# Performance work log

Hardware: AMD Instinct MI355X
Metric: run time of the kernel (lower is better)

The kernel has to match this reference:

```python
import jax, jax.numpy as jnp
import numpy as np


def setup_inputs() -> dict:
    key = jax.random.key(0)
    k1, k2, k3, k4 = jax.random.split(key, 4)
    B, L, D_IN, D_OUT, E = 512, 50, 768, 300, 8
    x = jax.random.normal(k1, (B, L, D_IN), dtype=jnp.float32)
    w_gate = jax.random.normal(k2, (D_IN, E), dtype=jnp.float32) * 0.02
    expert_w = jax.random.normal(k3, (E, D_OUT, D_IN), dtype=jnp.float32) * 0.02
    expert_bias = jax.random.normal(k4, (E, L, D_IN), dtype=jnp.float32) * 0.02
    return {"x": x, "w_gate": w_gate, "expert_w": expert_w, "expert_bias": expert_bias}


def reference(x, w_gate, expert_w, expert_bias):
    # Gating (eval mode: noisy gating disabled) -> softmax over experts
    gates = jax.nn.softmax(x @ w_gate, axis=-1)  # [B, L, E]
    # DTRLayer: lin(x - bias) = x @ W^T - bias @ W^T (linearity avoids [B,L,E,D_in] intermediate)
    xw = jnp.einsum('bli,eoi->bleo', x, expert_w)           # [B, L, E, O]
    bw = jnp.einsum('eli,eoi->leo', expert_bias, expert_w)  # [L, E, O]
    expert_out = xw - bw[None]                              # [B, L, E, O]
    # Gate-weighted sum over experts
    return jnp.einsum('ble,bleo->blo', gates, expert_out)   # [B, L, O]
```

## Files before the change

kernel.cpp:

```cpp
#include <hip/hip_runtime.h>
#include <hip/hip_bf16.h>

#define BATCH   512
#define LSEQ    50
#define DIN     768
#define DOUT    300
#define NEXP    8
#define NTOK    (BATCH * LSEQ)

typedef __bf16 bf16_t;
typedef __attribute__((ext_vector_type(8))) __bf16 bf16x8;
typedef __attribute__((ext_vector_type(4))) float f32x4;

#define GLDS16(g, l) __builtin_amdgcn_global_load_lds( \
    (__attribute__((address_space(1))) void*)(g), \
    (__attribute__((address_space(3))) void*)(l), 16, 0, 0)

static __device__ __forceinline__ unsigned short f2bf(float f) {
    unsigned u = __float_as_uint(f);
    u = (u + 0x7fff + ((u >> 16) & 1)) >> 16;
    return (unsigned short)u;
}

#define PREP_GATE_BLOCKS (NTOK / 4)
#define PREP_BW_BLOCKS   ((2 * NEXP * DOUT) / 4)

__global__ __launch_bounds__(256) void prep_kernel(
    const float* __restrict__ x, const float* __restrict__ wg,
    const float* __restrict__ bias, const float* __restrict__ W,
    unsigned short* __restrict__ xb, float* __restrict__ gates,
    float* __restrict__ bw, unsigned short* __restrict__ wb)
{
    const int tid  = threadIdx.x;
    const int lane = tid & 63;

    if (blockIdx.x < PREP_GATE_BLOCKS) {
        __shared__ float wgT[NEXP][DIN + 4];
        #pragma unroll
        for (int r = 0; r < 6; ++r) {
            int j = tid + 256 * r;
            float4 v = ((const float4*)wg)[j];
            int i  = j >> 1;
            int e0 = (j & 1) * 4;
            wgT[e0 + 0][i] = v.x;
            wgT[e0 + 1][i] = v.y;
            wgT[e0 + 2][i] = v.z;
            wgT[e0 + 3][i] = v.w;
        }
        __syncthreads();

        int t = blockIdx.x * 4 + (tid >> 6);
        const float4* xr = (const float4*)(x + (size_t)t * DIN);
        ushort4* xo = (ushort4*)(xb + (size_t)t * DIN);

        float acc[NEXP];
        #pragma unroll
        for (int e = 0; e < NEXP; e++) acc[e] = 0.0f;

        #pragma unroll
        for (int k = 0; k < 3; ++k) {
            int i4 = lane + 64 * k;
            float4 v = xr[i4];
            ushort4 u;
            u.x = f2bf(v.x); u.y = f2bf(v.y); u.z = f2bf(v.z); u.w = f2bf(v.w);
            xo[i4] = u;
            #pragma unroll
            for (int e = 0; e < NEXP; ++e) {
                float4 wv = *(const float4*)&wgT[e][4 * i4];
                acc[e] += v.x * wv.x + v.y * wv.y + v.z * wv.z + v.w * wv.w;
            }
        }
        #pragma unroll
        for (int e = 0; e < NEXP; e++) {
            #pragma unroll
            for (int m = 32; m > 0; m >>= 1) acc[e] += __shfl_xor(acc[e], m, 64);
        }
        float mx = acc[0];
        #pragma unroll
        for (int e = 1; e < NEXP; e++) mx = fmaxf(mx, acc[e]);
        float ex[NEXP]; float s = 0.0f;
        #pragma unroll
        for (int e = 0; e < NEXP; e++) { ex[e] = __expf(acc[e] - mx); s += ex[e]; }
        float inv = 1.0f / s;
        if (lane == 0) {
            #pragma unroll
            for (int e = 0; e < NEXP; e++) gates[(size_t)t * NEXP + e] = ex[e] * inv;
        }
    } else {
        int wid  = (blockIdx.x - PREP_GATE_BLOCKS) * 4 + (tid >> 6);
        int half = wid & 1;
        int eo   = wid >> 1;
        int e = eo / DOUT, o = eo % DOUT;

        const float4* wr = (const float4*)(W + ((size_t)e * DOUT + o) * DIN);
        float4 w4[3];
        #pragma unroll
        for (int k = 0; k < 3; ++k) w4[k] = wr[lane + 64 * k];

        if (half == 0) {
            ushort4* wo = (ushort4*)(wb + ((size_t)e * DOUT + o) * DIN);
            #pragma unroll
            for (int k = 0; k < 3; ++k) {
                ushort4 u;
                u.x = f2bf(w4[k].x); u.y = f2bf(w4[k].y);
                u.z = f2bf(w4[k].z); u.w = f2bf(w4[k].w);
                wo[lane + 64 * k] = u;
            }
        }

        int l0 = 25 * half;
        for (int l = l0; l < l0 + 25; ++l) {
            const float4* br = (const float4*)(bias + ((size_t)e * LSEQ + l) * DIN);
            float acc = 0.0f;
            #pragma unroll
            for (int k = 0; k < 3; ++k) {
                float4 b = br[lane + 64 * k];
                acc += b.x * w4[k].x + b.y * w4[k].y + b.z * w4[k].z + b.w * w4[k].w;
            }
            #pragma unroll
            for (int m = 32; m > 0; m >>= 1) acc += __shfl_xor(acc, m, 64);
            if (lane == 0) bw[((size_t)l * NEXP + e) * DOUT + o] = acc;
        }
    }
}

#define GTM 256
#define GTO 16
#define GBK 32
#define GKIT (DIN / GBK)
#define NRT  (NTOK / GTM)
#define NOT  19
#define RPG  13

__global__ __launch_bounds__(256, 2) void moe_mfma_kernel(
    const bf16_t* __restrict__ xb, const bf16_t* __restrict__ wb,
    const float* __restrict__ gates, const float* __restrict__ bw,
    float* __restrict__ out)
{
    const int bid  = blockIdx.x;
    const int g    = bid & 7;
    const int slot = bid >> 3;
    const int r_in = slot / NOT;
    const int o_t  = slot - NOT * r_in;
    const int r_t  = g * RPG + r_in;
    if (r_t >= NRT) return;
    const int o0 = o_t * GTO;
    const int t0 = r_t * GTM;

    __shared__ f32x4 ldsv[1536];
    char* Xs = (char*)ldsv;
    char* Ws = (char*)ldsv + 16384;

    const int tid  = threadIdx.x;
    const int w    = tid >> 6;
    const int lane = tid & 63;

    const int srow4 = lane >> 2;
    const int c16   = 16 * ((lane & 3) ^ ((lane >> 4) & 3));

    const char* xg[4];
    #pragma unroll
    for (int j = 0; j < 4; ++j)
        xg[j] = (const char*)xb + (size_t)(t0 + 64 * w + 16 * j + srow4) * (DIN * 2) + c16;
    char* xl = Xs + 4096 * w;

    const char* wg[2];
    #pragma unroll
    for (int j = 0; j < 2; ++j) {
        int n = 32 * w + 16 * j + srow4;
        int e = n >> 4;
        int o = o0 + (n & 15); if (o >= DOUT) o = DOUT - 1;
        wg[j] = (const char*)wb + (size_t)(e * DOUT + o) * (DIN * 2) + c16;
    }
    char* wl = Ws + 2048 * w;

    const int m = lane & 15, q = lane >> 4;
    const int sw = 16 * (q ^ ((m >> 2) & 3));
    int aoff[4], boff[8];
    #pragma unroll
    for (int rf = 0; rf < 4; ++rf) aoff[rf] = 64 * (64 * w + 16 * rf + m) + sw;
    #pragma unroll
    for (int cf = 0; cf < 8; ++cf) boff[cf] = 64 * (16 * cf + m) + sw;

    f32x4 acc[4][8] = {};

    for (int it = 0; it < GKIT; ++it) {
        #pragma unroll
        for (int j = 0; j < 4; ++j) GLDS16(xg[j], xl + 1024 * j);
        #pragma unroll
        for (int j = 0; j < 2; ++j) GLDS16(wg[j], wl + 1024 * j);
        #pragma unroll
        for (int j = 0; j < 4; ++j) xg[j] += 64;
        #pragma unroll
        for (int j = 0; j < 2; ++j) wg[j] += 64;
        __syncthreads();

        bf16x8 a[4];
        #pragma unroll
        for (int rf = 0; rf < 4; ++rf) a[rf] = *(const bf16x8*)(Xs + aoff[rf]);
        #pragma unroll
        for (int cf = 0; cf < 8; ++cf) {
            bf16x8 b = *(const bf16x8*)(Ws + boff[cf]);
            #pragma unroll
            for (int rf = 0; rf < 4; ++rf)
                acc[rf][cf] = __builtin_amdgcn_mfma_f32_16x16x32_bf16(a[rf], b, acc[rf][cf], 0, 0, 0);
        }
        __syncthreads();
    }

    const int o = o0 + m;
    if (o < DOUT) {
        #pragma unroll
        for (int rf = 0; rf < 4; ++rf) {
            #pragma unroll
            for (int r = 0; r < 4; ++r) {
                int t = t0 + 64 * w + 16 * rf + 4 * q + r;
                int l = t % LSEQ;
                float4 g0 = *(const float4*)(gates + (size_t)t * NEXP);
                float4 g1 = *(const float4*)(gates + (size_t)t * NEXP + 4);
                const float* bp = bw + (size_t)l * NEXP * DOUT + o;
                float s = 0.0f;
                s += g0.x * (acc[rf][0][r] - bp[0 * DOUT]);
                s += g0.y * (acc[rf][1][r] - bp[1 * DOUT]);
                s += g0.z * (acc[rf][2][r] - bp[2 * DOUT]);
                s += g0.w * (acc[rf][3][r] - bp[3 * DOUT]);
                s += g1.x * (acc[rf][4][r] - bp[4 * DOUT]);
                s += g1.y * (acc[rf][5][r] - bp[5 * DOUT]);
                s += g1.z * (acc[rf][6][r] - bp[6 * DOUT]);
                s += g1.w * (acc[rf][7][r] - bp[7 * DOUT]);
                out[(size_t)t * DOUT + o] = s;
            }
        }
    }
}

__global__ __launch_bounds__(256) void gates_kernel(
    const float* __restrict__ x, const float* __restrict__ wg,
    float* __restrict__ gates)
{
    int t    = blockIdx.x * 4 + (threadIdx.x >> 6);
    int lane = threadIdx.x & 63;
    const float* xr = x + (size_t)t * DIN;
    float acc[NEXP];
    #pragma unroll
    for (int e = 0; e < NEXP; e++) acc[e] = 0.0f;
    for (int i = lane; i < DIN; i += 64) {
        float xv = xr[i];
        const float* wr = wg + (size_t)i * NEXP;
        #pragma unroll
        for (int e = 0; e < NEXP; e++) acc[e] += xv * wr[e];
    }
    #pragma unroll
    for (int e = 0; e < NEXP; e++) {
        #pragma unroll
        for (int m = 32; m > 0; m >>= 1) acc[e] += __shfl_xor(acc[e], m, 64);
    }
    float mx = acc[0];
    #pragma unroll
    for (int e = 1; e < NEXP; e++) mx = fmaxf(mx, acc[e]);
    float ex[NEXP]; float s = 0.0f;
    #pragma unroll
    for (int e = 0; e < NEXP; e++) { ex[e] = __expf(acc[e] - mx); s += ex[e]; }
    float inv = 1.0f / s;
    if (lane == 0) {
        #pragma unroll
        for (int e = 0; e < NEXP; e++) gates[(size_t)t * NEXP + e] = ex[e] * inv;
    }
}

__global__ __launch_bounds__(256) void bw_kernel(
    const float* __restrict__ bias, const float* __restrict__ W,
    float* __restrict__ bw)
{
    int wave = blockIdx.x * 4 + (threadIdx.x >> 6);
    int lane = threadIdx.x & 63;
    int l   = wave / (NEXP * DOUT);
    int rem = wave % (NEXP * DOUT);
    int e   = rem / DOUT;
    int o   = rem % DOUT;
    const float4* br = (const float4*)(bias + ((size_t)e * LSEQ + l) * DIN);
    const float4* wr = (const float4*)(W    + ((size_t)e * DOUT + o) * DIN);
    float acc = 0.0f;
    #pragma unroll
    for (int k = 0; k < 3; ++k) {
        int i4 = lane + 64 * k;
        float4 b = br[i4], w = wr[i4];
        acc += b.x * w.x + b.y * w.y + b.z * w.z + b.w * w.w;
    }
    #pragma unroll
    for (int m = 32; m > 0; m >>= 1) acc += __shfl_xor(acc, m, 64);
    if (lane == 0) bw[((size_t)l * NEXP + e) * DOUT + o] = acc;
}

#define TM  64
#define TO  16
#define KT  32
#define KTP 36

__global__ __launch_bounds__(256) void moe_main_kernel(
    const float* __restrict__ x, const float* __restrict__ W,
    const float* __restrict__ gates, const float* __restrict__ bw,
    float* __restrict__ out)
{
    __shared__ float Xs[TM][KTP];
    __shared__ float Wls[128][KTP];
    const int tid = threadIdx.x;
    const int t0 = blockIdx.x * TM;
    const int o0 = blockIdx.y * TO;
    const int cg = tid & 15;
    const int tg = tid >> 4;
    const int lrow = tid >> 3;
    const int lk4  = (tid & 7) * 4;
    float acc[4][NEXP];
    #pragma unroll
    for (int i = 0; i < 4; i++)
        #pragma unroll
        for (int j = 0; j < NEXP; j++) acc[i][j] = 0.0f;
    for (int k0 = 0; k0 < DIN; k0 += KT) {
        #pragma unroll
        for (int r = 0; r < 2; r++) {
            int row = lrow + 32 * r;
            float4 v = *(const float4*)&x[((size_t)(t0 + row)) * DIN + k0 + lk4];
            *(float4*)&Xs[row][lk4] = v;
        }
        #pragma unroll
        for (int r = 0; r < 4; r++) {
            int nl = lrow + 32 * r;
            int e  = nl >> 4;
            int o  = o0 + (nl & 15);
            float4 v;
            if (o < DOUT)
                v = *(const float4*)&W[((size_t)e * DOUT + o) * DIN + k0 + lk4];
            else
                v = make_float4(0.f, 0.f, 0.f, 0.f);
            *(float4*)&Wls[nl][lk4] = v;
        }
        __syncthreads();
        #pragma unroll
        for (int k4 = 0; k4 < KT; k4 += 4) {
            float4 xa[4], wb4[NEXP];
            #pragma unroll
            for (int i = 0; i < 4; i++)
                xa[i] = *(const float4*)&Xs[tg + 16 * i][k4];
            #pragma unroll
            for (int j = 0; j < NEXP; j++)
                wb4[j] = *(const float4*)&Wls[cg + 16 * j][k4];
            #pragma unroll
            for (int i = 0; i < 4; i++)
                #pragma unroll
                for (int j = 0; j < NEXP; j++) {
                    acc[i][j] += xa[i].x * wb4[j].x;
                    acc[i][j] += xa[i].y * wb4[j].y;
                    acc[i][j] += xa[i].z * wb4[j].z;
                    acc[i][j] += xa[i].w * wb4[j].w;
                }
        }
        __syncthreads();
    }
    const int o = o0 + cg;
    if (o < DOUT) {
        #pragma unroll
        for (int i = 0; i < 4; i++) {
            int t = t0 + tg + 16 * i;
            int l = t % LSEQ;
            float s = 0.0f;
            #pragma unroll
            for (int j = 0; j < NEXP; j++) {
                float g = gates[(size_t)t * NEXP + j];
                s += g * (acc[i][j] - bw[((size_t)l * NEXP + j) * DOUT + o]);
            }
            out[(size_t)t * DOUT + o] = s;
        }
    }
}

extern "C" void kernel_launch(void* const* d_in, const int* in_sizes, int n_in,
                              void* d_out, int out_size, void* d_ws, size_t ws_size,
                              hipStream_t stream) {
    const float* x     = (const float*)d_in[0];
    const float* wgate = (const float*)d_in[1];
    const float* ew    = (const float*)d_in[2];
    const float* ebias = (const float*)d_in[3];
    float* out = (float*)d_out;

    const size_t n_gates = (size_t)NTOK * NEXP;
    const size_t n_bw    = (size_t)LSEQ * NEXP * DOUT;
    const size_t n_x     = (size_t)NTOK * DIN;
    const size_t n_w     = (size_t)NEXP * DOUT * DIN;

    float* gates = (float*)d_ws;
    float* bw    = gates + n_gates;
    bf16_t* xb   = (bf16_t*)(bw + n_bw);
    bf16_t* wbuf = xb + n_x;

    const size_t need = (n_gates + n_bw) * 4 + (n_x + n_w) * 2;

    if (ws_size >= need) {
        prep_kernel<<<PREP_GATE_BLOCKS + PREP_BW_BLOCKS, 256, 0, stream>>>(
            x, wgate, ebias, ew, (unsigned short*)xb, gates, bw, (unsigned short*)wbuf);
        moe_mfma_kernel<<<8 * RPG * NOT, 256, 0, stream>>>(xb, wbuf, gates, bw, out);
    } else {
        gates_kernel<<<NTOK / 4, 256, 0, stream>>>(x, wgate, gates);
        bw_kernel<<<(LSEQ * NEXP * DOUT) / 4, 256, 0, stream>>>(ebias, ew, bw);
        dim3 grid(NTOK / TM, (DOUT + TO - 1) / TO);
        moe_main_kernel<<<grid, 256, 0, stream>>>(x, ew, gates, bw, out);
    }
}
```

Before: 267.4 us.

## Fuse prep and MFMA GEMM into one cooperative persistent kernel with grid sync

Merges the gating/bf16-conversion/bias-projection prep stage and the bf16 MFMA GEMM into a single cooperative kernel of 512 persistent blocks. A grid-wide sync separates the two phases, and both phases iterate over work units with grid-stride loops. The goal is to remove the second kernel launch and the gap between kernels. The cost is a grid barrier, possible load imbalance from the fixed grid size, and fewer blocks in flight during the GEMM phase than the previous 1976-block launch. If the cooperative launch fails, the code falls back to the original two-kernel path.

```diff
diff --git a/kernel.cpp b/kernel.cpp
--- a/kernel.cpp
+++ b/kernel.cpp
@@ -1,5 +1,8 @@
 #include <hip/hip_runtime.h>
 #include <hip/hip_bf16.h>
+#include <hip/hip_cooperative_groups.h>
+
+namespace cg = cooperative_groups;
 
 #define BATCH   512
 #define LSEQ    50
@@ -20,6 +23,226 @@
     unsigned u = __float_as_uint(f);
     u = (u + 0x7fff + ((u >> 16) & 1)) >> 16;
     return (unsigned short)u;
+}
+
+#define GTM 256
+#define GTO 16
+#define GBK 32
+#define GKIT (DIN / GBK)
+#define NRT  (NTOK / GTM)
+#define NOT  19
+#define RPG  13
+#define NSLOT (8 * RPG * NOT)
+
+#define FUSED_GRID 512
+#define NUNITS (6400 + 4800)
+
+__global__ __launch_bounds__(256, 2) void fused_moe_kernel(
+    const float* __restrict__ x, const float* __restrict__ wgp,
+    const float* __restrict__ bias, const float* __restrict__ W,
+    unsigned short* __restrict__ xbu, float* __restrict__ gates,
+    float* __restrict__ bw, unsigned short* __restrict__ wbu,
+    float* __restrict__ out)
+{
+    __shared__ __align__(16) float wgT[NEXP][DIN + 4];
+
+    const int tid  = threadIdx.x;
+    const int lane = tid & 63;
+    const int w    = tid >> 6;
+
+    #pragma unroll
+    for (int r = 0; r < 6; ++r) {
+        int j = tid + 256 * r;
+        float4 v = ((const float4*)wgp)[j];
+        int i  = j >> 1;
+        int e0 = (j & 1) * 4;
+        wgT[e0 + 0][i] = v.x;
+        wgT[e0 + 1][i] = v.y;
+        wgT[e0 + 2][i] = v.z;
+        wgT[e0 + 3][i] = v.w;
+    }
+    __syncthreads();
+
+    const int gw = blockIdx.x * 4 + w;
+    for (int u = gw; u < NUNITS; u += FUSED_GRID * 4) {
+        if (u < 6400) {
+            const int tb = u * 4;
+            for (int tk = 0; tk < 4; ++tk) {
+                const int t = tb + tk;
+                const float4* xr = (const float4*)(x + (size_t)t * DIN);
+                ushort4*      xo = (ushort4*)(xbu + (size_t)t * DIN);
+
+                float acc[NEXP];
+                #pragma unroll
+                for (int e = 0; e < NEXP; e++) acc[e] = 0.0f;
+
+                #pragma unroll
+                for (int k = 0; k < 3; ++k) {
+                    int i4 = lane + 64 * k;
+                    float4 v = xr[i4];
+                    ushort4 uu;
+                    uu.x = f2bf(v.x); uu.y = f2bf(v.y);
+                    uu.z = f2bf(v.z); uu.w = f2bf(v.w);
+                    xo[i4] = uu;
+                    #pragma unroll
+                    for (int e = 0; e < NEXP; ++e) {
+                        float4 wv = *(const float4*)&wgT[e][4 * i4];
+                        acc[e] += v.x * wv.x + v.y * wv.y + v.z * wv.z + v.w * wv.w;
+                    }
+                }
+                #pragma unroll
+                for (int e = 0; e < NEXP; e++) {
+                    #pragma unroll
+                    for (int m2 = 32; m2 > 0; m2 >>= 1)
+                        acc[e] += __shfl_xor(acc[e], m2, 64);
+                }
+                float mx = acc[0];
+                #pragma unroll
+                for (int e = 1; e < NEXP; e++) mx = fmaxf(mx, acc[e]);
+                float ex[NEXP]; float s = 0.0f;
+                #pragma unroll
+                for (int e = 0; e < NEXP; e++) { ex[e] = __expf(acc[e] - mx); s += ex[e]; }
+                float inv = 1.0f / s;
+                if (lane == 0) {
+                    *(float4*)(gates + (size_t)t * NEXP) =
+                        make_float4(ex[0]*inv, ex[1]*inv, ex[2]*inv, ex[3]*inv);
+                    *(float4*)(gates + (size_t)t * NEXP + 4) =
+                        make_float4(ex[4]*inv, ex[5]*inv, ex[6]*inv, ex[7]*inv);
+                }
+            }
+        } else {
+            const int wid  = u - 6400;
+            const int half = wid & 1;
+            const int eo   = wid >> 1;
+            const int e = eo / DOUT, o = eo % DOUT;
+
+            const float4* wr = (const float4*)(W + ((size_t)e * DOUT + o) * DIN);
+            float4 w4[3];
+            #pragma unroll
+            for (int k = 0; k < 3; ++k) w4[k] = wr[lane + 64 * k];
+
+            if (half == 0) {
+                ushort4* wo = (ushort4*)(wbu + ((size_t)e * DOUT + o) * DIN);
+                #pragma unroll
+                for (int k = 0; k < 3; ++k) {
+                    ushort4 uu;
+                    uu.x = f2bf(w4[k].x); uu.y = f2bf(w4[k].y);
+                    uu.z = f2bf(w4[k].z); uu.w = f2bf(w4[k].w);
+                    wo[lane + 64 * k] = uu;
+                }
+            }
+
+            int l0 = 25 * half;
+            for (int l = l0; l < l0 + 25; ++l) {
+                const float4* br = (const float4*)(bias + ((size_t)e * LSEQ + l) * DIN);
+                float acc = 0.0f;
+                #pragma unroll
+                for (int k = 0; k < 3; ++k) {
+                    float4 b = br[lane + 64 * k];
+                    acc += b.x * w4[k].x + b.y * w4[k].y + b.z * w4[k].z + b.w * w4[k].w;
+                }
+                #pragma unroll
+                for (int m2 = 32; m2 > 0; m2 >>= 1) acc += __shfl_xor(acc, m2, 64);
+                if (lane == 0) bw[((size_t)l * NEXP + e) * DOUT + o] = acc;
+            }
+        }
+    }
+
+    cg::this_grid().sync();
+
+    char* Xs = (char*)wgT;
+    char* Ws = (char*)wgT + 16384;
+
+    const int srow4 = lane >> 2;
+    const int c16   = 16 * ((lane & 3) ^ ((lane >> 4) & 3));
+    const int m = lane & 15, q = lane >> 4;
+    const int sw = 16 * (q ^ ((m >> 2) & 3));
+    int aoff[4], boff[8];
+    #pragma unroll
+    for (int rf = 0; rf < 4; ++rf) aoff[rf] = 64 * (64 * w + 16 * rf + m) + sw;
+    #pragma unroll
+    for (int cf = 0; cf < 8; ++cf) boff[cf] = 64 * (16 * cf + m) + sw;
+
+    const bf16_t* xb = (const bf16_t*)xbu;
+    const bf16_t* wb = (const bf16_t*)wbu;
+
+    for (int vb = blockIdx.x; vb < NSLOT; vb += FUSED_GRID) {
+        const int g    = vb & 7;
+        const int slot = vb >> 3;
+        const int r_in = slot / NOT;
+        const int o_t  = slot - NOT * r_in;
+        const int r_t  = g * RPG + r_in;
+        if (r_t >= NRT) continue;
+        const int o0 = o_t * GTO;
+        const int t0 = r_t * GTM;
+
+        const char* xg[4];
+        #pragma unroll
+        for (int j = 0; j < 4; ++j)
+            xg[j] = (const char*)xb + (size_t)(t0 + 64 * w + 16 * j + srow4) * (DIN * 2) + c16;
+        char* xl = Xs + 4096 * w;
+
+        const char* wq[2];
+        #pragma unroll
+        for (int j = 0; j < 2; ++j) {
+            int n = 32 * w + 16 * j + srow4;
+            int e = n >> 4;
+            int o = o0 + (n & 15); if (o >= DOUT) o = DOUT - 1;
+            wq[j] = (const char*)wb + (size_t)(e * DOUT + o) * (DIN * 2) + c16;
+        }
+        char* wl = Ws + 2048 * w;
+
+        f32x4 acc[4][8] = {};
+
+        for (int it = 0; it < GKIT; ++it) {
+            #pragma unroll
+            for (int j = 0; j < 4; ++j) GLDS16(xg[j], xl + 1024 * j);
+            #pragma unroll
+            for (int j = 0; j < 2; ++j) GLDS16(wq[j], wl + 1024 * j);
+            #pragma unroll
+            for (int j = 0; j < 4; ++j) xg[j] += 64;
+            #pragma unroll
+            for (int j = 0; j < 2; ++j) wq[j] += 64;
+            __syncthreads();
+
+            bf16x8 a[4];
+            #pragma unroll
+            for (int rf = 0; rf < 4; ++rf) a[rf] = *(const bf16x8*)(Xs + aoff[rf]);
+            #pragma unroll
+            for (int cf = 0; cf < 8; ++cf) {
+                bf16x8 b = *(const bf16x8*)(Ws + boff[cf]);
+                #pragma unroll
+                for (int rf = 0; rf < 4; ++rf)
+                    acc[rf][cf] = __builtin_amdgcn_mfma_f32_16x16x32_bf16(a[rf], b, acc[rf][cf], 0, 0, 0);
+            }
+            __syncthreads();
+        }
+
+        const int o = o0 + m;
+        if (o < DOUT) {
+            #pragma unroll
+            for (int rf = 0; rf < 4; ++rf) {
+                #pragma unroll
+                for (int r = 0; r < 4; ++r) {
+                    int t = t0 + 64 * w + 16 * rf + 4 * q + r;
+                    int l = t % LSEQ;
+                    float4 g0 = *(const float4*)(gates + (size_t)t * NEXP);
+                    float4 g1 = *(const float4*)(gates + (size_t)t * NEXP + 4);
+                    const float* bp = bw + (size_t)l * NEXP * DOUT + o;
+                    float s = 0.0f;
+                    s += g0.x * (acc[rf][0][r] - bp[0 * DOUT]);
+                    s += g0.y * (acc[rf][1][r] - bp[1 * DOUT]);
+                    s += g0.z * (acc[rf][2][r] - bp[2 * DOUT]);
+                    s += g0.w * (acc[rf][3][r] - bp[3 * DOUT]);
+                    s += g1.x * (acc[rf][4][r] - bp[4 * DOUT]);
+                    s += g1.y * (acc[rf][5][r] - bp[5 * DOUT]);
+                    s += g1.z * (acc[rf][6][r] - bp[6 * DOUT]);
+                    s += g1.w * (acc[rf][7][r] - bp[7 * DOUT]);
+                    out[(size_t)t * DOUT + o] = s;
+                }
+            }
+        }
+    }
 }
 
 #define PREP_GATE_BLOCKS (NTOK / 4)
@@ -123,14 +346,6 @@
         }
     }
 }
-
-#define GTM 256
-#define GTO 16
-#define GBK 32
-#define GKIT (DIN / GBK)
-#define NRT  (NTOK / GTM)
-#define NOT  19
-#define RPG  13
 
 __global__ __launch_bounds__(256, 2) void moe_mfma_kernel(
     const bf16_t* __restrict__ xb, const bf16_t* __restrict__ wb,
@@ -307,7 +522,7 @@
     const int tid = threadIdx.x;
     const int t0 = blockIdx.x * TM;
     const int o0 = blockIdx.y * TO;
-    const int cg = tid & 15;
+    const int cg2 = tid & 15;
     const int tg = tid >> 4;
     const int lrow = tid >> 3;
     const int lk4  = (tid & 7) * 4;
@@ -344,7 +559,7 @@
                 xa[i] = *(const float4*)&Xs[tg + 16 * i][k4];
             #pragma unroll
             for (int j = 0; j < NEXP; j++)
-                wb4[j] = *(const float4*)&Wls[cg + 16 * j][k4];
+                wb4[j] = *(const float4*)&Wls[cg2 + 16 * j][k4];
             #pragma unroll
             for (int i = 0; i < 4; i++)
                 #pragma unroll
@@ -357,7 +572,7 @@
         }
         __syncthreads();
     }
-    const int o = o0 + cg;
+    const int o = o0 + cg2;
     if (o < DOUT) {
         #pragma unroll
         for (int i = 0; i < 4; i++) {
@@ -396,9 +611,19 @@
     const size_t need = (n_gates + n_bw) * 4 + (n_x + n_w) * 2;
 
     if (ws_size >= need) {
-        prep_kernel<<<PREP_GATE_BLOCKS + PREP_BW_BLOCKS, 256, 0, stream>>>(
-            x, wgate, ebias, ew, (unsigned short*)xb, gates, bw, (unsigned short*)wbuf);
-        moe_mfma_kernel<<<8 * RPG * NOT, 256, 0, stream>>>(xb, wbuf, gates, bw, out);
+        unsigned short* xbu = (unsigned short*)xb;
+        unsigned short* wbu = (unsigned short*)wbuf;
+        void* kargs[] = {
+            (void*)&x, (void*)&wgate, (void*)&ebias, (void*)&ew,
+            (void*)&xbu, (void*)&gates, (void*)&bw, (void*)&wbu, (void*)&out
+        };
+        hipError_t cerr = hipLaunchCooperativeKernel(
+            fused_moe_kernel, dim3(FUSED_GRID), dim3(256), kargs, 0u, stream);
+        if (cerr != hipSuccess) {
+            prep_kernel<<<PREP_GATE_BLOCKS + PREP_BW_BLOCKS, 256, 0, stream>>>(
+                x, wgate, ebias, ew, (unsigned short*)xb, gates, bw, (unsigned short*)wbuf);
+            moe_mfma_kernel<<<NSLOT, 256, 0, stream>>>(xb, wbuf, gates, bw, out);
+        }
     } else {
         gates_kernel<<<NTOK / 4, 256, 0, stream>>>(x, wgate, gates);
         bw_kernel<<<(LSEQ * NEXP * DOUT) / 4, 256, 0, stream>>>(ebias, ew, bw);
```

After: 379.6 us. +42.0%, slower.

## Use 512-thread blocks with triple-buffered LDS pipeline in MoE MFMA GEMM

Applied to the files above, without the earlier changes.

Replaces the 256-thread, single-buffered GEMM loop with a 512-thread block covering 512 tokens, a three-stage LDS ring (prefetch two K-steps ahead) and split load/compute phases with explicit waitcnt, barriers and setprio. The aim is to hide global-to-LDS latency behind MFMA work and halve redundant weight-tile loads per token. In exchange it needs 120KB of LDS per block, which may limit occupancy, and relies on exact vmcnt accounting for correctness. The epilogue is unchanged apart from the indexing rework.

```diff
diff --git a/kernel.cpp b/kernel.cpp
--- a/kernel.cpp
+++ b/kernel.cpp
@@ -124,15 +124,15 @@
     }
 }
 
-#define GTM 256
-#define GTO 16
-#define GBK 32
-#define GKIT (DIN / GBK)
-#define NRT  (NTOK / GTM)
-#define NOT  19
-#define RPG  13
-
-__global__ __launch_bounds__(256, 2) void moe_mfma_kernel(
+#define BM8   512
+#define NRT8  (NTOK / BM8)
+#define NOT8  19
+#define RPG8  7
+#define NSLOT8 (8 * RPG8 * NOT8)
+#define KTN   (DIN / 32)
+#define TBUF  40960
+
+__global__ __launch_bounds__(512, 2) void moe_mfma8_kernel(
     const bf16_t* __restrict__ xb, const bf16_t* __restrict__ wb,
     const float* __restrict__ gates, const float* __restrict__ bw,
     float* __restrict__ out)
@@ -140,16 +140,14 @@
     const int bid  = blockIdx.x;
     const int g    = bid & 7;
     const int slot = bid >> 3;
-    const int r_in = slot / NOT;
-    const int o_t  = slot - NOT * r_in;
-    const int r_t  = g * RPG + r_in;
-    if (r_t >= NRT) return;
-    const int o0 = o_t * GTO;
-    const int t0 = r_t * GTM;
-
-    __shared__ f32x4 ldsv[1536];
-    char* Xs = (char*)ldsv;
-    char* Ws = (char*)ldsv + 16384;
+    const int r_in = slot / NOT8;
+    const int o_t  = slot - NOT8 * r_in;
+    const int r_t  = g * RPG8 + r_in;
+    if (r_t >= NRT8) return;
+    const int o0 = o_t * 16;
+    const int t0 = r_t * BM8;
+
+    __shared__ __align__(16) char lds[3 * TBUF];
 
     const int tid  = threadIdx.x;
     const int w    = tid >> 6;
@@ -158,54 +156,110 @@
     const int srow4 = lane >> 2;
     const int c16   = 16 * ((lane & 3) ^ ((lane >> 4) & 3));
 
-    const char* xg[4];
-    #pragma unroll
-    for (int j = 0; j < 4; ++j)
-        xg[j] = (const char*)xb + (size_t)(t0 + 64 * w + 16 * j + srow4) * (DIN * 2) + c16;
-    char* xl = Xs + 4096 * w;
-
-    const char* wg[2];
-    #pragma unroll
-    for (int j = 0; j < 2; ++j) {
-        int n = 32 * w + 16 * j + srow4;
+    const char* xga[4];
+    #pragma unroll
+    for (int r = 0; r < 4; ++r)
+        xga[r] = (const char*)xb + (size_t)(t0 + r * 128 + w * 16 + srow4) * (DIN * 2) + c16;
+
+    const char* wga;
+    {
+        int n = w * 16 + srow4;
         int e = n >> 4;
         int o = o0 + (n & 15); if (o >= DOUT) o = DOUT - 1;
-        wg[j] = (const char*)wb + (size_t)(e * DOUT + o) * (DIN * 2) + c16;
-    }
-    char* wl = Ws + 2048 * w;
+        wga = (const char*)wb + (size_t)(e * DOUT + o) * (DIN * 2) + c16;
+    }
 
     const int m = lane & 15, q = lane >> 4;
     const int sw = 16 * (q ^ ((m >> 2) & 3));
     int aoff[4], boff[8];
     #pragma unroll
-    for (int rf = 0; rf < 4; ++rf) aoff[rf] = 64 * (64 * w + 16 * rf + m) + sw;
-    #pragma unroll
-    for (int cf = 0; cf < 8; ++cf) boff[cf] = 64 * (16 * cf + m) + sw;
+    for (int rf = 0; rf < 4; ++rf) aoff[rf] = (w * 64 + rf * 16 + m) * 64 + sw;
+    #pragma unroll
+    for (int cf = 0; cf < 8; ++cf) boff[cf] = 32768 + (cf * 16 + m) * 64 + sw;
 
     f32x4 acc[4][8] = {};
 
-    for (int it = 0; it < GKIT; ++it) {
-        #pragma unroll
-        for (int j = 0; j < 4; ++j) GLDS16(xg[j], xl + 1024 * j);
-        #pragma unroll
-        for (int j = 0; j < 2; ++j) GLDS16(wg[j], wl + 1024 * j);
-        #pragma unroll
-        for (int j = 0; j < 4; ++j) xg[j] += 64;
-        #pragma unroll
-        for (int j = 0; j < 2; ++j) wg[j] += 64;
-        __syncthreads();
-
-        bf16x8 a[4];
-        #pragma unroll
-        for (int rf = 0; rf < 4; ++rf) a[rf] = *(const bf16x8*)(Xs + aoff[rf]);
-        #pragma unroll
-        for (int cf = 0; cf < 8; ++cf) {
-            bf16x8 b = *(const bf16x8*)(Ws + boff[cf]);
-            #pragma unroll
-            for (int rf = 0; rf < 4; ++rf)
-                acc[rf][cf] = __builtin_amdgcn_mfma_f32_16x16x32_bf16(a[rf], b, acc[rf][cf], 0, 0, 0);
-        }
-        __syncthreads();
+    #pragma unroll
+    for (int r = 0; r < 4; ++r) GLDS16(xga[r], lds + r * 8192 + w * 1024);
+    GLDS16(wga, lds + 32768 + w * 1024);
+    #pragma unroll
+    for (int r = 0; r < 4; ++r) GLDS16(xga[r] + 64, lds + TBUF + r * 8192 + w * 1024);
+    GLDS16(wga + 64, lds + TBUF + 32768 + w * 1024);
+
+    int cbuf = 0;
+    for (int j = 0; j < KTN; ++j) {
+        int s = j + 2; if (s >= KTN) s -= KTN;
+        const int koff = s * 64;
+        int sbuf = cbuf + 2; if (sbuf >= 3) sbuf -= 3;
+        char* sb = lds + sbuf * TBUF;
+        const char* cb = lds + cbuf * TBUF;
+
+        GLDS16(xga[0] + koff, sb + 0 * 8192 + w * 1024);
+        GLDS16(xga[1] + koff, sb + 1 * 8192 + w * 1024);
+        GLDS16(xga[2] + koff, sb + 2 * 8192 + w * 1024);
+        asm volatile("s_waitcnt vmcnt(8)" ::: "memory");
+        __builtin_amdgcn_s_barrier();
+        __builtin_amdgcn_sched_barrier(0);
+
+        bf16x8 b0 = *(const bf16x8*)(cb + boff[0]);
+        bf16x8 b1 = *(const bf16x8*)(cb + boff[1]);
+        bf16x8 b2 = *(const bf16x8*)(cb + boff[2]);
+        bf16x8 b3 = *(const bf16x8*)(cb + boff[3]);
+        bf16x8 b4 = *(const bf16x8*)(cb + boff[4]);
+        bf16x8 b5 = *(const bf16x8*)(cb + boff[5]);
+        bf16x8 b6 = *(const bf16x8*)(cb + boff[6]);
+        bf16x8 b7 = *(const bf16x8*)(cb + boff[7]);
+        bf16x8 a0 = *(const bf16x8*)(cb + aoff[0]);
+        bf16x8 a1 = *(const bf16x8*)(cb + aoff[1]);
+        asm volatile("s_waitcnt lgkmcnt(0)" ::: "memory");
+        __builtin_amdgcn_sched_barrier(0);
+        __builtin_amdgcn_s_setprio(1);
+        acc[0][0] = __builtin_amdgcn_mfma_f32_16x16x32_bf16(a0, b0, acc[0][0], 0, 0, 0);
+        acc[0][1] = __builtin_amdgcn_mfma_f32_16x16x32_bf16(a0, b1, acc[0][1], 0, 0, 0);
+        acc[0][2] = __builtin_amdgcn_mfma_f32_16x16x32_bf16(a0, b2, acc[0][2], 0, 0, 0);
+        acc[0][3] = __builtin_amdgcn_mfma_f32_16x16x32_bf16(a0, b3, acc[0][3], 0, 0, 0);
+        acc[0][4] = __builtin_amdgcn_mfma_f32_16x16x32_bf16(a0, b4, acc[0][4], 0, 0, 0);
+        acc[0][5] = __builtin_amdgcn_mfma_f32_16x16x32_bf16(a0, b5, acc[0][5], 0, 0, 0);
+        acc[0][6] = __builtin_amdgcn_mfma_f32_16x16x32_bf16(a0, b6, acc[0][6], 0, 0, 0);
+        acc[0][7] = __builtin_amdgcn_mfma_f32_16x16x32_bf16(a0, b7, acc[0][7], 0, 0, 0);
+        acc[1][0] = __builtin_amdgcn_mfma_f32_16x16x32_bf16(a1, b0, acc[1][0], 0, 0, 0);
+        acc[1][1] = __builtin_amdgcn_mfma_f32_16x16x32_bf16(a1, b1, acc[1][1], 0, 0, 0);
+        acc[1][2] = __builtin_amdgcn_mfma_f32_16x16x32_bf16(a1, b2, acc[1][2], 0, 0, 0);
+        acc[1][3] = __builtin_amdgcn_mfma_f32_16x16x32_bf16(a1, b3, acc[1][3], 0, 0, 0);
+        acc[1][4] = __builtin_amdgcn_mfma_f32_16x16x32_bf16(a1, b4, acc[1][4], 0, 0, 0);
+        acc[1][5] = __builtin_amdgcn_mfma_f32_16x16x32_bf16(a1, b5, acc[1][5], 0, 0, 0);
+        acc[1][6] = __builtin_amdgcn_mfma_f32_16x16x32_bf16(a1, b6, acc[1][6], 0, 0, 0);
+        acc[1][7] = __builtin_amdgcn_mfma_f32_16x16x32_bf16(a1, b7, acc[1][7], 0, 0, 0);
+        __builtin_amdgcn_s_setprio(0);
+        __builtin_amdgcn_s_barrier();
+
+        GLDS16(xga[3] + koff, sb + 3 * 8192 + w * 1024);
+        GLDS16(wga + koff, sb + 32768 + w * 1024);
+        bf16x8 a2 = *(const bf16x8*)(cb + aoff[2]);
+        bf16x8 a3 = *(const bf16x8*)(cb + aoff[3]);
+        asm volatile("s_waitcnt lgkmcnt(0)" ::: "memory");
+        __builtin_amdgcn_sched_barrier(0);
+        __builtin_amdgcn_s_setprio(1);
+        acc[2][0] = __builtin_amdgcn_mfma_f32_16x16x32_bf16(a2, b0, acc[2][0], 0, 0, 0);
+        acc[2][1] = __builtin_amdgcn_mfma_f32_16x16x32_bf16(a2, b1, acc[2][1], 0, 0, 0);
+        acc[2][2] = __builtin_amdgcn_mfma_f32_16x16x32_bf16(a2, b2, acc[2][2], 0, 0, 0);
+        acc[2][3] = __builtin_amdgcn_mfma_f32_16x16x32_bf16(a2, b3, acc[2][3], 0, 0, 0);
+        acc[2][4] = __builtin_amdgcn_mfma_f32_16x16x32_bf16(a2, b4, acc[2][4], 0, 0, 0);
+        acc[2][5] = __builtin_amdgcn_mfma_f32_16x16x32_bf16(a2, b5, acc[2][5], 0, 0, 0);
+        acc[2][6] = __builtin_amdgcn_mfma_f32_16x16x32_bf16(a2, b6, acc[2][6], 0, 0, 0);
+        acc[2][7] = __builtin_amdgcn_mfma_f32_16x16x32_bf16(a2, b7, acc[2][7], 0, 0, 0);
+        acc[3][0] = __builtin_amdgcn_mfma_f32_16x16x32_bf16(a3, b0, acc[3][0], 0, 0, 0);
+        acc[3][1] = __builtin_amdgcn_mfma_f32_16x16x32_bf16(a3, b1, acc[3][1], 0, 0, 0);
+        acc[3][2] = __builtin_amdgcn_mfma_f32_16x16x32_bf16(a3, b2, acc[3][2], 0, 0, 0);
+        acc[3][3] = __builtin_amdgcn_mfma_f32_16x16x32_bf16(a3, b3, acc[3][3], 0, 0, 0);
+        acc[3][4] = __builtin_amdgcn_mfma_f32_16x16x32_bf16(a3, b4, acc[3][4], 0, 0, 0);
+        acc[3][5] = __builtin_amdgcn_mfma_f32_16x16x32_bf16(a3, b5, acc[3][5], 0, 0, 0);
+        acc[3][6] = __builtin_amdgcn_mfma_f32_16x16x32_bf16(a3, b6, acc[3][6], 0, 0, 0);
+        acc[3][7] = __builtin_amdgcn_mfma_f32_16x16x32_bf16(a3, b7, acc[3][7], 0, 0, 0);
+        __builtin_amdgcn_s_setprio(0);
+        __builtin_amdgcn_s_barrier();
+
+        cbuf += 1; if (cbuf >= 3) cbuf -= 3;
     }
 
     const int o = o0 + m;
@@ -398,7 +452,7 @@
     if (ws_size >= need) {
         prep_kernel<<<PREP_GATE_BLOCKS + PREP_BW_BLOCKS, 256, 0, stream>>>(
             x, wgate, ebias, ew, (unsigned short*)xb, gates, bw, (unsigned short*)wbuf);
-        moe_mfma_kernel<<<8 * RPG * NOT, 256, 0, stream>>>(xb, wbuf, gates, bw, out);
+        moe_mfma8_kernel<<<NSLOT8, 512, 0, stream>>>(xb, wbuf, gates, bw, out);
     } else {
         gates_kernel<<<NTOK / 4, 256, 0, stream>>>(x, wgate, gates);
         bw_kernel<<<(LSEQ * NEXP * DOUT) / 4, 256, 0, stream>>>(ebias, ew, bw);
```

New measurement: 296.3 us. 10.8% more time.

## Load A fragments directly to registers and double-buffer W tiles in LDS

Applied to the files above, without the earlier changes.

The X (A operand) tile now goes straight from global memory into registers, with register double-buffering, instead of being staged through LDS. The W (B operand) tile is double-buffered in LDS, so the load for the next k-step is issued while the current step's MFMAs run. This cuts the two barriers per iteration to one and shrinks LDS use, aiming to hide global-load latency behind compute. In exchange it relies on hand-placed waitcnt and sched_barrier calls, and the direct global loads of A may be less coalesced than the LDS-staged path.

```diff
diff --git a/kernel.cpp b/kernel.cpp
--- a/kernel.cpp
+++ b/kernel.cpp
@@ -126,11 +126,81 @@
 
 #define GTM 256
 #define GTO 16
-#define GBK 32
-#define GKIT (DIN / GBK)
+#define GKIT (DIN / 32)
 #define NRT  (NTOK / GTM)
 #define NOT  19
 #define RPG  13
+#define NSLOT (8 * RPG * NOT)
+#define BBUF 8192
+
+#define MFMA32(A0, A1, A2, A3)                                                      \
+    acc[0][0] = __builtin_amdgcn_mfma_f32_16x16x32_bf16(A0, b0, acc[0][0], 0, 0, 0); \
+    acc[0][1] = __builtin_amdgcn_mfma_f32_16x16x32_bf16(A0, b1, acc[0][1], 0, 0, 0); \
+    acc[0][2] = __builtin_amdgcn_mfma_f32_16x16x32_bf16(A0, b2, acc[0][2], 0, 0, 0); \
+    acc[0][3] = __builtin_amdgcn_mfma_f32_16x16x32_bf16(A0, b3, acc[0][3], 0, 0, 0); \
+    acc[0][4] = __builtin_amdgcn_mfma_f32_16x16x32_bf16(A0, b4, acc[0][4], 0, 0, 0); \
+    acc[0][5] = __builtin_amdgcn_mfma_f32_16x16x32_bf16(A0, b5, acc[0][5], 0, 0, 0); \
+    acc[0][6] = __builtin_amdgcn_mfma_f32_16x16x32_bf16(A0, b6, acc[0][6], 0, 0, 0); \
+    acc[0][7] = __builtin_amdgcn_mfma_f32_16x16x32_bf16(A0, b7, acc[0][7], 0, 0, 0); \
+    acc[1][0] = __builtin_amdgcn_mfma_f32_16x16x32_bf16(A1, b0, acc[1][0], 0, 0, 0); \
+    acc[1][1] = __builtin_amdgcn_mfma_f32_16x16x32_bf16(A1, b1, acc[1][1], 0, 0, 0); \
+    acc[1][2] = __builtin_amdgcn_mfma_f32_16x16x32_bf16(A1, b2, acc[1][2], 0, 0, 0); \
+    acc[1][3] = __builtin_amdgcn_mfma_f32_16x16x32_bf16(A1, b3, acc[1][3], 0, 0, 0); \
+    acc[1][4] = __builtin_amdgcn_mfma_f32_16x16x32_bf16(A1, b4, acc[1][4], 0, 0, 0); \
+    acc[1][5] = __builtin_amdgcn_mfma_f32_16x16x32_bf16(A1, b5, acc[1][5], 0, 0, 0); \
+    acc[1][6] = __builtin_amdgcn_mfma_f32_16x16x32_bf16(A1, b6, acc[1][6], 0, 0, 0); \
+    acc[1][7] = __builtin_amdgcn_mfma_f32_16x16x32_bf16(A1, b7, acc[1][7], 0, 0, 0); \
+    acc[2][0] = __builtin_amdgcn_mfma_f32_16x16x32_bf16(A2, b0, acc[2][0], 0, 0, 0); \
+    acc[2][1] = __builtin_amdgcn_mfma_f32_16x16x32_bf16(A2, b1, acc[2][1], 0, 0, 0); \
+    acc[2][2] = __builtin_amdgcn_mfma_f32_16x16x32_bf16(A2, b2, acc[2][2], 0, 0, 0); \
+    acc[2][3] = __builtin_amdgcn_mfma_f32_16x16x32_bf16(A2, b3, acc[2][3], 0, 0, 0); \
+    acc[2][4] = __builtin_amdgcn_mfma_f32_16x16x32_bf16(A2, b4, acc[2][4], 0, 0, 0); \
+    acc[2][5] = __builtin_amdgcn_mfma_f32_16x16x32_bf16(A2, b5, acc[2][5], 0, 0, 0); \
+    acc[2][6] = __builtin_amdgcn_mfma_f32_16x16x32_bf16(A2, b6, acc[2][6], 0, 0, 0); \
+    acc[2][7] = __builtin_amdgcn_mfma_f32_16x16x32_bf16(A2, b7, acc[2][7], 0, 0, 0); \
+    acc[3][0] = __builtin_amdgcn_mfma_f32_16x16x32_bf16(A3, b0, acc[3][0], 0, 0, 0); \
+    acc[3][1] = __builtin_amdgcn_mfma_f32_16x16x32_bf16(A3, b1, acc[3][1], 0, 0, 0); \
+    acc[3][2] = __builtin_amdgcn_mfma_f32_16x16x32_bf16(A3, b2, acc[3][2], 0, 0, 0); \
+    acc[3][3] = __builtin_amdgcn_mfma_f32_16x16x32_bf16(A3, b3, acc[3][3], 0, 0, 0); \
+    acc[3][4] = __builtin_amdgcn_mfma_f32_16x16x32_bf16(A3, b4, acc[3][4], 0, 0, 0); \
+    acc[3][5] = __builtin_amdgcn_mfma_f32_16x16x32_bf16(A3, b5, acc[3][5], 0, 0, 0); \
+    acc[3][6] = __builtin_amdgcn_mfma_f32_16x16x32_bf16(A3, b6, acc[3][6], 0, 0, 0); \
+    acc[3][7] = __builtin_amdgcn_mfma_f32_16x16x32_bf16(A3, b7, acc[3][7], 0, 0, 0);
+
+#define KBODY(J, AU0, AU1, AU2, AU3, AL0, AL1, AL2, AL3) do {                  \
+    const int jj  = (J);                                                       \
+    const int cur = jj & 1;                                                    \
+    if (jj + 1 < GKIT) {                                                       \
+        AL0 = *(const bf16x8*)(xga[0]);                                        \
+        AL1 = *(const bf16x8*)(xga[1]);                                        \
+        AL2 = *(const bf16x8*)(xga[2]);                                        \
+        AL3 = *(const bf16x8*)(xga[3]);                                        \
+        xga[0] += 64; xga[1] += 64; xga[2] += 64; xga[3] += 64;                \
+        asm volatile("s_waitcnt vmcnt(4)" ::: "memory");         \
+    } else {                                                                   \
+        asm volatile("s_waitcnt vmcnt(0)" ::: "memory");       \
+    }                                                                          \
+    __builtin_amdgcn_s_barrier();             \
+    __builtin_amdgcn_sched_barrier(0);                                         \
+    if (jj + 1 < GKIT) {                                                       \
+        char* nb = lds + BBUF * (cur ^ 1);                                     \
+        GLDS16(wq[0], nb + 2048 * w);                                          \
+        GLDS16(wq[1], nb + 2048 * w + 1024);                                   \
+        wq[0] += 64; wq[1] += 64;                                              \
+    }                                                                          \
+    const char* cb = lds + BBUF * cur;                                         \
+    bf16x8 b0 = *(const bf16x8*)(cb + boff[0]);                                \
+    bf16x8 b1 = *(const bf16x8*)(cb + boff[1]);                                \
+    bf16x8 b2 = *(const bf16x8*)(cb + boff[2]);                                \
+    bf16x8 b3 = *(const bf16x8*)(cb + boff[3]);                                \
+    bf16x8 b4 = *(const bf16x8*)(cb + boff[4]);                                \
+    bf16x8 b5 = *(const bf16x8*)(cb + boff[5]);                                \
+    bf16x8 b6 = *(const bf16x8*)(cb + boff[6]);                                \
+    bf16x8 b7 = *(const bf16x8*)(cb + boff[7]);                                \
+    asm volatile("s_waitcnt lgkmcnt(0)" ::: "memory");                         \
+    __builtin_amdgcn_sched_barrier(0);                                         \
+    MFMA32(AU0, AU1, AU2, AU3)                                                 \
+} while (0)
 
 __global__ __launch_bounds__(256, 2) void moe_mfma_kernel(
     const bf16_t* __restrict__ xb, const bf16_t* __restrict__ wb,
@@ -147,9 +217,7 @@
     const int o0 = o_t * GTO;
     const int t0 = r_t * GTM;
 
-    __shared__ f32x4 ldsv[1536];
-    char* Xs = (char*)ldsv;
-    char* Ws = (char*)ldsv + 16384;
+    __shared__ __align__(16) char lds[2 * BBUF];
 
     const int tid  = threadIdx.x;
     const int w    = tid >> 6;
@@ -158,54 +226,42 @@
     const int srow4 = lane >> 2;
     const int c16   = 16 * ((lane & 3) ^ ((lane >> 4) & 3));
 
-    const char* xg[4];
-    #pragma unroll
-    for (int j = 0; j < 4; ++j)
-        xg[j] = (const char*)xb + (size_t)(t0 + 64 * w + 16 * j + srow4) * (DIN * 2) + c16;
-    char* xl = Xs + 4096 * w;
-
-    const char* wg[2];
+    const char* wq[2];
     #pragma unroll
     for (int j = 0; j < 2; ++j) {
         int n = 32 * w + 16 * j + srow4;
         int e = n >> 4;
         int o = o0 + (n & 15); if (o >= DOUT) o = DOUT - 1;
-        wg[j] = (const char*)wb + (size_t)(e * DOUT + o) * (DIN * 2) + c16;
-    }
-    char* wl = Ws + 2048 * w;
+        wq[j] = (const char*)wb + (size_t)(e * DOUT + o) * (DIN * 2) + c16;
+    }
 
     const int m = lane & 15, q = lane >> 4;
     const int sw = 16 * (q ^ ((m >> 2) & 3));
-    int aoff[4], boff[8];
-    #pragma unroll
-    for (int rf = 0; rf < 4; ++rf) aoff[rf] = 64 * (64 * w + 16 * rf + m) + sw;
-    #pragma unroll
-    for (int cf = 0; cf < 8; ++cf) boff[cf] = 64 * (16 * cf + m) + sw;
+    int boff[8];
+    #pragma unroll
+    for (int cf = 0; cf < 8; ++cf) boff[cf] = (16 * cf + m) * 64 + sw;
+
+    const char* xga[4];
+    #pragma unroll
+    for (int rf = 0; rf < 4; ++rf)
+        xga[rf] = (const char*)xb + (size_t)(t0 + 64 * w + 16 * rf + m) * (DIN * 2) + q * 16;
 
     f32x4 acc[4][8] = {};
 
-    for (int it = 0; it < GKIT; ++it) {
-        #pragma unroll
-        for (int j = 0; j < 4; ++j) GLDS16(xg[j], xl + 1024 * j);
-        #pragma unroll
-        for (int j = 0; j < 2; ++j) GLDS16(wg[j], wl + 1024 * j);
-        #pragma unroll
-        for (int j = 0; j < 4; ++j) xg[j] += 64;
-        #pragma unroll
-        for (int j = 0; j < 2; ++j) wg[j] += 64;
-        __syncthreads();
-
-        bf16x8 a[4];
-        #pragma unroll
-        for (int rf = 0; rf < 4; ++rf) a[rf] = *(const bf16x8*)(Xs + aoff[rf]);
-        #pragma unroll
-        for (int cf = 0; cf < 8; ++cf) {
-            bf16x8 b = *(const bf16x8*)(Ws + boff[cf]);
-            #pragma unroll
-            for (int rf = 0; rf < 4; ++rf)
-                acc[rf][cf] = __builtin_amdgcn_mfma_f32_16x16x32_bf16(a[rf], b, acc[rf][cf], 0, 0, 0);
-        }
-        __syncthreads();
+    GLDS16(wq[0], lds + 2048 * w);
+    GLDS16(wq[1], lds + 2048 * w + 1024);
+    wq[0] += 64; wq[1] += 64;
+
+    bf16x8 aC0 = *(const bf16x8*)(xga[0]);
+    bf16x8 aC1 = *(const bf16x8*)(xga[1]);
+    bf16x8 aC2 = *(const bf16x8*)(xga[2]);
+    bf16x8 aC3 = *(const bf16x8*)(xga[3]);
+    xga[0] += 64; xga[1] += 64; xga[2] += 64; xga[3] += 64;
+    bf16x8 aN0, aN1, aN2, aN3;
+
+    for (int it = 0; it < GKIT; it += 2) {
+        KBODY(it,     aC0, aC1, aC2, aC3, aN0, aN1, aN2, aN3);
+        KBODY(it + 1, aN0, aN1, aN2, aN3, aC0, aC1, aC2, aC3);
     }
 
     const int o = o0 + m;
@@ -398,7 +454,7 @@
     if (ws_size >= need) {
         prep_kernel<<<PREP_GATE_BLOCKS + PREP_BW_BLOCKS, 256, 0, stream>>>(
             x, wgate, ebias, ew, (unsigned short*)xb, gates, bw, (unsigned short*)wbuf);
-        moe_mfma_kernel<<<8 * RPG * NOT, 256, 0, stream>>>(xb, wbuf, gates, bw, out);
+        moe_mfma_kernel<<<NSLOT, 256, 0, stream>>>(xb, wbuf, gates, bw, out);
     } else {
         gates_kernel<<<NTOK / 4, 256, 0, stream>>>(x, wgate, gates);
         bw_kernel<<<(LSEQ * NEXP * DOUT) / 4, 256, 0, stream>>>(ebias, ew, bw);
```

Result: slower. 285.5 us (+6.8%).
